# Kernel optimization log

Measured on AMD Instinct MI355X. Metric: run time of the kernel, lower is better.

## Reference

```python
import jax, jax.numpy as jnp
import numpy as np

N = 100000      # nodes (single node type)
E = 400000      # edges per relation
R = 4           # relations
DIN = 128       # h_dim
H1 = 8          # heads, layer 1
DH1 = DIN // H1 # per-head dim, layer 1
DOUT = 128      # out_dim (layer 2 has 1 head of dim DOUT)
NEG_SLOPE = 0.2 # GATConv default leaky_relu slope


def gat_rel_layer(h, src, dst, W, al, ar, loop_w, bias, activation):
    """One RelationalAttLayer: per-relation GATConv (bias=False), summed across
    relations, + self-loop matmul + bias + optional relu. dropout=0.
    h: [N, din]; src/dst: [R, E]; W: [R, din, H*Dh]; al/ar: [R, H, Dh];
    loop_w: [din, dout]; bias: [dout]."""
    n = h.shape[0]

    def per_rel(src_r, dst_r, W_r, al_r, ar_r):
        nh, dh = al_r.shape
        Wh = (h @ W_r).reshape(n, nh, dh)                 # [N,H,Dh]
        el = jnp.sum(Wh * al_r, axis=-1)                  # [N,H]
        er = jnp.sum(Wh * ar_r, axis=-1)                  # [N,H]
        e = jax.nn.leaky_relu(el[src_r] + er[dst_r], NEG_SLOPE)  # [E,H]
        # edge-softmax over incoming edges per destination node (stable)
        m = jax.lax.stop_gradient(jax.ops.segment_max(e, dst_r, num_segments=n))
        ex = jnp.exp(e - m[dst_r])
        denom = jax.ops.segment_sum(ex, dst_r, num_segments=n)  # [N,H]
        alpha = ex / denom[dst_r]                                # [E,H]
        # scatter-aggregate messages
        return jax.ops.segment_sum(alpha[:, :, None] * Wh[src_r], dst_r,
                                   num_segments=n)               # [N,H,Dh]

    outs = jax.vmap(per_rel)(src, dst, W, al, ar)  # [R,N,H,Dh]
    hout = outs.sum(0).reshape(n, -1)              # cross-relation sum, flatten heads
    hout = hout + h @ loop_w + bias                # self-loop + h_bias
    if activation:
        hout = jax.nn.relu(hout)
    return hout


def setup_inputs() -> dict:
    key = jax.random.key(0)
    ks = jax.random.split(key, 14)
    s = 0.1
    return {
        "h": jax.random.normal(ks[0], (N, DIN), dtype=jnp.float32),
        "src_idx": jax.random.randint(ks[1], (R, E), 0, N, dtype=jnp.int32),
        "dst_idx": jax.random.randint(ks[2], (R, E), 0, N, dtype=jnp.int32),
        # layer 1 params (h_dim -> h_dim, H1 heads)
        "W1": jax.random.normal(ks[3], (R, DIN, H1 * DH1), dtype=jnp.float32) * s,
        "al1": jax.random.normal(ks[4], (R, H1, DH1), dtype=jnp.float32) * s,
        "ar1": jax.random.normal(ks[5], (R, H1, DH1), dtype=jnp.float32) * s,
        "loop1": jax.random.normal(ks[6], (DIN, DIN), dtype=jnp.float32) * s,
        "b1": jnp.zeros((DIN,), dtype=jnp.float32),
        # layer 2 params (h_dim -> out_dim, 1 head)
        "W2": jax.random.normal(ks[7], (R, DIN, DOUT), dtype=jnp.float32) * s,
        "al2": jax.random.normal(ks[8], (R, 1, DOUT), dtype=jnp.float32) * s,
        "ar2": jax.random.normal(ks[9], (R, 1, DOUT), dtype=jnp.float32) * s,
        "loop2": jax.random.normal(ks[10], (DIN, DOUT), dtype=jnp.float32) * s,
        "b2": jnp.zeros((DOUT,), dtype=jnp.float32),
    }


def reference(h, src_idx, dst_idx, W1, al1, ar1, loop1, b1,
              W2, al2, ar2, loop2, b2):
    # hidden layer: relu activation; last layer: no activation (last_layer_act=False)
    h1 = gat_rel_layer(h, src_idx, dst_idx, W1, al1, ar1, loop1, b1, activation=True)
    h2 = gat_rel_layer(h1, src_idx, dst_idx, W2, al2, ar2, loop2, b2, activation=False)
    return h2
```

## Files before the change

### kernel.cpp

```cpp
#include <hip/hip_runtime.h>

#define NN 100000
#define NE 400000
#define NREL 4
#define MAXDEG 24

typedef unsigned short u16;
typedef __attribute__((ext_vector_type(8))) short bf16x8;
typedef __attribute__((ext_vector_type(4))) float f32x4;

__device__ __forceinline__ u16 f2bf(float x) {
    union { float f; unsigned int u; } v; v.f = x;
    unsigned int r = v.u + 0x7fffu + ((v.u >> 16) & 1u);
    return (u16)(r >> 16);
}
__device__ __forceinline__ float bf2f(u16 x) {
    union { unsigned int u; float f; } v; v.u = ((unsigned int)x) << 16;
    return v.f;
}

template <bool RELU>
__global__ __launch_bounds__(256) void conv_kernel(
    const float* __restrict__ X, u16* __restrict__ Xb, int n8)
{
    int i = blockIdx.x * 256 + threadIdx.x;
    if (i >= n8) return;
    float4 a = ((const float4*)X)[2 * i];
    float4 b = ((const float4*)X)[2 * i + 1];
    if (RELU) {
        a.x = fmaxf(a.x, 0.f); a.y = fmaxf(a.y, 0.f);
        a.z = fmaxf(a.z, 0.f); a.w = fmaxf(a.w, 0.f);
        b.x = fmaxf(b.x, 0.f); b.y = fmaxf(b.y, 0.f);
        b.z = fmaxf(b.z, 0.f); b.w = fmaxf(b.w, 0.f);
    }
    ushort4 lo, hi;
    lo.x = f2bf(a.x); lo.y = f2bf(a.y); lo.z = f2bf(a.z); lo.w = f2bf(a.w);
    hi.x = f2bf(b.x); hi.y = f2bf(b.y); hi.z = f2bf(b.z); hi.w = f2bf(b.w);
    ((ushort4*)Xb)[2 * i] = lo;
    ((ushort4*)Xb)[2 * i + 1] = hi;
}

__global__ __launch_bounds__(256) void build_b_kernel(
    const float* __restrict__ W, const float* __restrict__ loopw,
    u16* __restrict__ Bb)
{
    int id = blockIdx.x * 256 + threadIdx.x;
    if (id >= 5 * 16384) return;
    int j = id >> 14, rem = id & 16383;
    int c = rem >> 7, k = rem & 127;
    const float* M = (j < 4) ? (W + j * 16384) : loopw;
    Bb[id] = f2bf(M[k * 128 + c]);
}

__global__ __launch_bounds__(256) void build_w_kernel(
    const float* __restrict__ W, const float* __restrict__ al,
    const float* __restrict__ ar, u16* __restrict__ wcatB,
    int nh, int dh, int PC)
{
    int id = blockIdx.x * 256 + threadIdx.x;
    if (id >= PC * 128) return;
    int j = id >> 7, k = id & 127;
    int P2 = 8 * nh;
    float s = 0.f;
    if (j < P2) {
        int half = 4 * nh;
        int jj = (j < half) ? j : j - half;
        const float* av = (j < half) ? al : ar;
        int r = jj / nh, h = jj % nh;
        for (int i = 0; i < dh; ++i)
            s += W[r * 16384 + k * 128 + h * dh + i] * av[(r * nh + h) * dh + i];
    }
    wcatB[j * 128 + k] = f2bf(s);
}

__global__ __launch_bounds__(256) void csr_build_kernel(
    const int* __restrict__ src, const int* __restrict__ dst,
    int* __restrict__ cur, int* __restrict__ bucket)
{
    int i = blockIdx.x * 256 + threadIdx.x;
    if (i >= NREL * NE) return;
    int d = dst[i], s = src[i];
    int r = i / NE;
    int pos = atomicAdd(&cur[r * NN + d], 1);
    if (pos < MAXDEG) bucket[((size_t)r * NN + d) * MAXDEG + pos] = s;
}

__device__ __forceinline__ void stage_and_mfma(
    const u16* __restrict__ Xb, const u16* __restrict__ B, int row0, int n,
    u16 (*sA)[136], u16 (*sB)[136], f32x4 acc[8], int tid)
{
#pragma unroll
    for (int i = 0; i < 8; ++i) {
        int idx = tid + 256 * i;
        int r = idx >> 4, ch = idx & 15;
        *(float4*)&sB[r][ch * 8] = ((const float4*)B)[idx];
    }
#pragma unroll
    for (int i = 0; i < 4; ++i) {
        int idx = tid + 256 * i;
        int r = idx >> 4, ch = idx & 15;
        int gr = row0 + r;
        float4 v = make_float4(0.f, 0.f, 0.f, 0.f);
        if (gr < n) v = *(const float4*)(Xb + (size_t)gr * 128 + ch * 8);
        *(float4*)&sA[r][ch * 8] = v;
    }
    __syncthreads();

    const int w = tid >> 6, lane = tid & 63;
    const int lr = lane & 15, hi = lane >> 4;
#pragma unroll
    for (int fn = 0; fn < 8; ++fn) acc[fn] = (f32x4){0.f, 0.f, 0.f, 0.f};
#pragma unroll
    for (int ko = 0; ko < 4; ++ko) {
        const int kk = ko * 32 + hi * 8;
        bf16x8 a = *(const bf16x8*)&sA[w * 16 + lr][kk];
#pragma unroll
        for (int fn = 0; fn < 8; ++fn) {
            bf16x8 b = *(const bf16x8*)&sB[fn * 16 + lr][kk];
            acc[fn] = __builtin_amdgcn_mfma_f32_16x16x32_bf16(a, b, acc[fn], 0, 0, 0);
        }
    }
}

__global__ __launch_bounds__(256) void gemm_rel_kernel(
    const u16* __restrict__ Xb, const u16* __restrict__ Bb, int rbase,
    u16* __restrict__ Wh, int n)
{
    __shared__ u16 sA[64][136];
    __shared__ u16 sB[128][136];
    const int tid = threadIdx.x;
    const int row0 = blockIdx.x * 64;
    f32x4 acc[8];
    stage_and_mfma(Xb, Bb + (size_t)(rbase + blockIdx.y) * 16384, row0, n, sA, sB, acc, tid);

    const int w = tid >> 6, lane = tid & 63;
    const int lr = lane & 15, hi = lane >> 4;
    u16* Wr = Wh + (size_t)blockIdx.y * NN * 128;
#pragma unroll
    for (int reg = 0; reg < 4; ++reg) {
        int grow = row0 + w * 16 + hi * 4 + reg;
        if (grow >= n) continue;
        u16* crow = Wr + (size_t)grow * 128;
#pragma unroll
        for (int fn = 0; fn < 8; ++fn)
            crow[fn * 16 + lr] = f2bf(acc[fn][reg]);
    }
}

__global__ __launch_bounds__(256) void gemm_loop_kernel(
    const u16* __restrict__ Xb, const u16* __restrict__ Bb,
    float* __restrict__ O, const float* __restrict__ bias, int n)
{
    __shared__ u16 sA[64][136];
    __shared__ u16 sB[128][136];
    const int tid = threadIdx.x;
    const int row0 = blockIdx.x * 64;
    f32x4 acc[8];
    stage_and_mfma(Xb, Bb + 4 * 16384, row0, n, sA, sB, acc, tid);

    const int w = tid >> 6, lane = tid & 63;
    const int lr = lane & 15, hi = lane >> 4;
#pragma unroll
    for (int reg = 0; reg < 4; ++reg) {
        int grow = row0 + w * 16 + hi * 4 + reg;
        if (grow >= n) continue;
        float* crow = O + (size_t)grow * 128;
#pragma unroll
        for (int fn = 0; fn < 8; ++fn) {
            int col = fn * 16 + lr;
            crow[col] = acc[fn][reg] + bias[col];
        }
    }
}

template <int NF>
__global__ __launch_bounds__(256) void elr_gemm_kernel(
    const u16* __restrict__ Xb, const u16* __restrict__ Bb,
    float* __restrict__ Eo, int P2, int n)
{
    __shared__ u16 sA[64][136];
    __shared__ u16 sB[NF * 16][136];
    const int tid = threadIdx.x;
    const int row0 = blockIdx.x * 64;

    for (int idx = tid; idx < NF * 256; idx += 256) {
        int r = idx >> 4, ch = idx & 15;
        *(float4*)&sB[r][ch * 8] = ((const float4*)Bb)[idx];
    }
#pragma unroll
    for (int i = 0; i < 4; ++i) {
        int idx = tid + 256 * i;
        int r = idx >> 4, ch = idx & 15;
        int gr = row0 + r;
        float4 v = make_float4(0.f, 0.f, 0.f, 0.f);
        if (gr < n) v = *(const float4*)(Xb + (size_t)gr * 128 + ch * 8);
        *(float4*)&sA[r][ch * 8] = v;
    }
    __syncthreads();

    const int w = tid >> 6, lane = tid & 63;
    const int lr = lane & 15, hi = lane >> 4;
    f32x4 acc[NF];
#pragma unroll
    for (int fn = 0; fn < NF; ++fn) acc[fn] = (f32x4){0.f, 0.f, 0.f, 0.f};
#pragma unroll
    for (int ko = 0; ko < 4; ++ko) {
        const int kk = ko * 32 + hi * 8;
        bf16x8 a = *(const bf16x8*)&sA[w * 16 + lr][kk];
#pragma unroll
        for (int fn = 0; fn < NF; ++fn) {
            bf16x8 b = *(const bf16x8*)&sB[fn * 16 + lr][kk];
            acc[fn] = __builtin_amdgcn_mfma_f32_16x16x32_bf16(a, b, acc[fn], 0, 0, 0);
        }
    }
#pragma unroll
    for (int reg = 0; reg < 4; ++reg) {
        int grow = row0 + w * 16 + hi * 4 + reg;
        if (grow >= n) continue;
#pragma unroll
        for (int fn = 0; fn < NF; ++fn) {
            int col = fn * 16 + lr;
            if (col < P2) Eo[(size_t)grow * P2 + col] = acc[fn][reg];
        }
    }
}

__global__ __launch_bounds__(256) void gather_kernel(
    const int* __restrict__ cnt, const int* __restrict__ bucket,
    const float* __restrict__ elr, const u16* __restrict__ Wh,
    float* __restrict__ O, int ST, int nh, int dh_shift, int r0, int nb)
{
    int d = blockIdx.x * 4 + (threadIdx.x >> 6);
    if (d >= NN) return;
    int lane = threadIdx.x & 63;
    int c0 = lane * 2;
    int hh = c0 >> dh_shift;
    float M0 = 0.f, M1 = 0.f;
    for (int rr = 0; rr < nb; ++rr) {
        int r = r0 + rr;
        int deg = cnt[r * NN + d];
        if (deg <= 0) continue;
        deg = deg > MAXDEG ? MAXDEG : deg;
        const int* bk = bucket + ((size_t)r * NN + d) * MAXDEG;
        float erd = elr[(size_t)d * ST + NREL * nh + r * nh + hh];
        const u16* whr = Wh + (size_t)rr * NN * 128;
        float dn = 0.f, m0 = 0.f, m1 = 0.f;
        for (int e = 0; e < deg; ++e) {
            int s = bk[e];
            float v = elr[(size_t)s * ST + r * nh + hh] + erd;
            v = v > 0.f ? v : 0.2f * v;
            float ex = __expf(v);
            dn += ex;
            ushort2 wv = *(const ushort2*)(whr + (size_t)s * 128 + c0);
            m0 = fmaf(ex, bf2f(wv.x), m0);
            m1 = fmaf(ex, bf2f(wv.y), m1);
        }
        float inv = 1.f / dn;
        M0 = fmaf(m0, inv, M0);
        M1 = fmaf(m1, inv, M1);
    }
    float2* op = (float2*)(O + (size_t)d * 128) + lane;
    float2 c = *op;
    c.x += M0; c.y += M1;
    *op = c;
}

static void run_layer(const u16* Xb, float* O, const float* W,
                      const float* al, const float* ar, const float* loopw,
                      const float* biasv, int nh, int dh, int dh_shift, int NF,
                      const int* cnt, const int* bucket,
                      u16* Wh, float* elr, u16* Bb, u16* wcatB, int nb,
                      hipStream_t stream)
{
    const int P2 = 8 * nh, PC = NF * 16;
    build_b_kernel<<<(5 * 16384) / 256, 256, 0, stream>>>(W, loopw, Bb);
    build_w_kernel<<<(PC * 128 + 255) / 256, 256, 0, stream>>>(W, al, ar, wcatB, nh, dh, PC);

    const int gg = (NN + 63) / 64;
    gemm_loop_kernel<<<gg, 256, 0, stream>>>(Xb, Bb, O, biasv, NN);
    if (NF == 4)
        elr_gemm_kernel<4><<<gg, 256, 0, stream>>>(Xb, wcatB, elr, P2, NN);
    else
        elr_gemm_kernel<1><<<gg, 256, 0, stream>>>(Xb, wcatB, elr, P2, NN);

    for (int r0 = 0; r0 < NREL; r0 += nb) {
        gemm_rel_kernel<<<dim3(gg, nb), 256, 0, stream>>>(Xb, Bb, r0, Wh, NN);
        gather_kernel<<<(NN + 3) / 4, 256, 0, stream>>>(
            cnt, bucket, elr, Wh, O, P2, nh, dh_shift, r0, nb);
    }
}

extern "C" void kernel_launch(void* const* d_in, const int* in_sizes, int n_in,
                              void* d_out, int out_size, void* d_ws, size_t ws_size,
                              hipStream_t stream)
{
    const float* h   = (const float*)d_in[0];
    const int*   src = (const int*)d_in[1];
    const int*   dst = (const int*)d_in[2];
    const float* W1  = (const float*)d_in[3];
    const float* al1 = (const float*)d_in[4];
    const float* ar1 = (const float*)d_in[5];
    const float* lp1 = (const float*)d_in[6];
    const float* b1  = (const float*)d_in[7];
    const float* W2  = (const float*)d_in[8];
    const float* al2 = (const float*)d_in[9];
    const float* ar2 = (const float*)d_in[10];
    const float* lp2 = (const float*)d_in[11];
    const float* b2  = (const float*)d_in[12];

    float* out = (float*)d_out;
    char*  p   = (char*)d_ws;

    const size_t szXb  = (size_t)NN * 128 * 2;
    const size_t szO   = (size_t)NN * 128 * 4;
    const size_t szElr = (size_t)NN * 64 * 4;
    const size_t szCnt = (size_t)NREL * NN * 4;
    const size_t szBkt = (size_t)NREL * NN * MAXDEG * 4;
    const size_t szBb  = 5 * 16384 * 2;
    const size_t szWc  = 64 * 128 * 2;
    const size_t szWh1 = (size_t)NN * 128 * 2;
    const size_t fixed = szXb + szO + szElr + szCnt + szBkt + szBb + szWc;

    int nb = 1;
    if (ws_size >= fixed + 4 * szWh1) nb = 4;
    else if (ws_size >= fixed + 2 * szWh1) nb = 2;

    u16*   Xb     = (u16*)p;    p += szXb;
    float* O1     = (float*)p;  p += szO;
    float* elr    = (float*)p;  p += szElr;
    int*   cnt    = (int*)p;    p += szCnt;
    int*   bucket = (int*)p;    p += szBkt;
    u16*   Bb     = (u16*)p;    p += szBb;
    u16*   wcatB  = (u16*)p;    p += szWc;
    u16*   Wh     = (u16*)p;

    hipMemsetAsync(cnt, 0, szCnt, stream);
    csr_build_kernel<<<(NREL * NE + 255) / 256, 256, 0, stream>>>(src, dst, cnt, bucket);

    const int n8 = NN * 128 / 8;
    conv_kernel<false><<<(n8 + 255) / 256, 256, 0, stream>>>(h, Xb, n8);
    run_layer(Xb, O1, W1, al1, ar1, lp1, b1, 8, 16, 4, 4,
              cnt, bucket, Wh, elr, Bb, wcatB, nb, stream);
    conv_kernel<true><<<(n8 + 255) / 256, 256, 0, stream>>>(O1, Xb, n8);
    run_layer(Xb, out, W2, al2, ar2, lp2, b2, 1, 128, 7, 1,
              cnt, bucket, Wh, elr, Bb, wcatB, nb, stream);
}
```

Measured before the change: 821.1 us.

## Fuse per-layer GEMMs into one launch and parallelize gather across relations

The relation, self-loop and attention-logit GEMMs now run in a single kernel with a 6-way grid y dimension, replacing several launches. The gather kernel gives each destination node its own block, with one wave per relation and a shared-memory reduction, and unrolls the edge loop by four with vectorized index loads. CSR construction handles all four relations per thread. The workspace-size fallback for fewer relation buffers is removed, so the code always assumes room for all four Wh buffers; this risks failure when the workspace is small, and the gather launches more, smaller blocks.

```diff
diff --git a/kernel.cpp b/kernel.cpp
--- a/kernel.cpp
+++ b/kernel.cpp
@@ -54,11 +54,10 @@
 
 __global__ __launch_bounds__(256) void build_w_kernel(
     const float* __restrict__ W, const float* __restrict__ al,
-    const float* __restrict__ ar, u16* __restrict__ wcatB,
-    int nh, int dh, int PC)
+    const float* __restrict__ ar, u16* __restrict__ wcatB, int nh, int dh)
 {
     int id = blockIdx.x * 256 + threadIdx.x;
-    if (id >= PC * 128) return;
+    if (id >= 16384) return;
     int j = id >> 7, k = id & 127;
     int P2 = 8 * nh;
     float s = 0.f;
@@ -78,22 +77,39 @@
     int* __restrict__ cur, int* __restrict__ bucket)
 {
     int i = blockIdx.x * 256 + threadIdx.x;
-    if (i >= NREL * NE) return;
-    int d = dst[i], s = src[i];
-    int r = i / NE;
-    int pos = atomicAdd(&cur[r * NN + d], 1);
-    if (pos < MAXDEG) bucket[((size_t)r * NN + d) * MAXDEG + pos] = s;
-}
-
-__device__ __forceinline__ void stage_and_mfma(
-    const u16* __restrict__ Xb, const u16* __restrict__ B, int row0, int n,
-    u16 (*sA)[136], u16 (*sB)[136], f32x4 acc[8], int tid)
-{
+    if (i >= NE) return;
+    int d0 = dst[i],          s0 = src[i];
+    int d1 = dst[NE + i],     s1 = src[NE + i];
+    int d2 = dst[2 * NE + i], s2 = src[2 * NE + i];
+    int d3 = dst[3 * NE + i], s3 = src[3 * NE + i];
+    int p0 = atomicAdd(&cur[d0], 1);
+    int p1 = atomicAdd(&cur[NN + d1], 1);
+    int p2 = atomicAdd(&cur[2 * NN + d2], 1);
+    int p3 = atomicAdd(&cur[3 * NN + d3], 1);
+    if (p0 < MAXDEG) bucket[(size_t)d0 * MAXDEG + p0] = s0;
+    if (p1 < MAXDEG) bucket[((size_t)NN + d1) * MAXDEG + p1] = s1;
+    if (p2 < MAXDEG) bucket[((size_t)2 * NN + d2) * MAXDEG + p2] = s2;
+    if (p3 < MAXDEG) bucket[((size_t)3 * NN + d3) * MAXDEG + p3] = s3;
+}
+
+__global__ __launch_bounds__(256) void fused_gemm_kernel(
+    const u16* __restrict__ Xb, const u16* __restrict__ Bb,
+    const u16* __restrict__ wcatB, u16* __restrict__ Wh,
+    float* __restrict__ O, const float* __restrict__ bias,
+    float* __restrict__ elr, int P2, int n)
+{
+    __shared__ u16 sA[64][136];
+    __shared__ u16 sB[128][136];
+    const int tid = threadIdx.x;
+    const int y = blockIdx.y;
+    const int row0 = blockIdx.x * 64;
+    const u16* Bmat = (y < 5) ? (Bb + (size_t)y * 16384) : wcatB;
+
 #pragma unroll
     for (int i = 0; i < 8; ++i) {
         int idx = tid + 256 * i;
         int r = idx >> 4, ch = idx & 15;
-        *(float4*)&sB[r][ch * 8] = ((const float4*)B)[idx];
+        *(float4*)&sB[r][ch * 8] = ((const float4*)Bmat)[idx];
     }
 #pragma unroll
     for (int i = 0; i < 4; ++i) {
@@ -108,6 +124,7 @@
 
     const int w = tid >> 6, lane = tid & 63;
     const int lr = lane & 15, hi = lane >> 4;
+    f32x4 acc[8];
 #pragma unroll
     for (int fn = 0; fn < 8; ++fn) acc[fn] = (f32x4){0.f, 0.f, 0.f, 0.f};
 #pragma unroll
@@ -120,107 +137,40 @@
             acc[fn] = __builtin_amdgcn_mfma_f32_16x16x32_bf16(a, b, acc[fn], 0, 0, 0);
         }
     }
-}
-
-__global__ __launch_bounds__(256) void gemm_rel_kernel(
-    const u16* __restrict__ Xb, const u16* __restrict__ Bb, int rbase,
-    u16* __restrict__ Wh, int n)
-{
-    __shared__ u16 sA[64][136];
-    __shared__ u16 sB[128][136];
-    const int tid = threadIdx.x;
-    const int row0 = blockIdx.x * 64;
-    f32x4 acc[8];
-    stage_and_mfma(Xb, Bb + (size_t)(rbase + blockIdx.y) * 16384, row0, n, sA, sB, acc, tid);
-
-    const int w = tid >> 6, lane = tid & 63;
-    const int lr = lane & 15, hi = lane >> 4;
-    u16* Wr = Wh + (size_t)blockIdx.y * NN * 128;
-#pragma unroll
-    for (int reg = 0; reg < 4; ++reg) {
-        int grow = row0 + w * 16 + hi * 4 + reg;
-        if (grow >= n) continue;
-        u16* crow = Wr + (size_t)grow * 128;
-#pragma unroll
-        for (int fn = 0; fn < 8; ++fn)
-            crow[fn * 16 + lr] = f2bf(acc[fn][reg]);
-    }
-}
-
-__global__ __launch_bounds__(256) void gemm_loop_kernel(
-    const u16* __restrict__ Xb, const u16* __restrict__ Bb,
-    float* __restrict__ O, const float* __restrict__ bias, int n)
-{
-    __shared__ u16 sA[64][136];
-    __shared__ u16 sB[128][136];
-    const int tid = threadIdx.x;
-    const int row0 = blockIdx.x * 64;
-    f32x4 acc[8];
-    stage_and_mfma(Xb, Bb + 4 * 16384, row0, n, sA, sB, acc, tid);
-
-    const int w = tid >> 6, lane = tid & 63;
-    const int lr = lane & 15, hi = lane >> 4;
-#pragma unroll
-    for (int reg = 0; reg < 4; ++reg) {
-        int grow = row0 + w * 16 + hi * 4 + reg;
-        if (grow >= n) continue;
-        float* crow = O + (size_t)grow * 128;
-#pragma unroll
-        for (int fn = 0; fn < 8; ++fn) {
-            int col = fn * 16 + lr;
-            crow[col] = acc[fn][reg] + bias[col];
-        }
-    }
-}
-
-template <int NF>
-__global__ __launch_bounds__(256) void elr_gemm_kernel(
-    const u16* __restrict__ Xb, const u16* __restrict__ Bb,
-    float* __restrict__ Eo, int P2, int n)
-{
-    __shared__ u16 sA[64][136];
-    __shared__ u16 sB[NF * 16][136];
-    const int tid = threadIdx.x;
-    const int row0 = blockIdx.x * 64;
-
-    for (int idx = tid; idx < NF * 256; idx += 256) {
-        int r = idx >> 4, ch = idx & 15;
-        *(float4*)&sB[r][ch * 8] = ((const float4*)Bb)[idx];
-    }
-#pragma unroll
-    for (int i = 0; i < 4; ++i) {
-        int idx = tid + 256 * i;
-        int r = idx >> 4, ch = idx & 15;
-        int gr = row0 + r;
-        float4 v = make_float4(0.f, 0.f, 0.f, 0.f);
-        if (gr < n) v = *(const float4*)(Xb + (size_t)gr * 128 + ch * 8);
-        *(float4*)&sA[r][ch * 8] = v;
-    }
-    __syncthreads();
-
-    const int w = tid >> 6, lane = tid & 63;
-    const int lr = lane & 15, hi = lane >> 4;
-    f32x4 acc[NF];
-#pragma unroll
-    for (int fn = 0; fn < NF; ++fn) acc[fn] = (f32x4){0.f, 0.f, 0.f, 0.f};
-#pragma unroll
-    for (int ko = 0; ko < 4; ++ko) {
-        const int kk = ko * 32 + hi * 8;
-        bf16x8 a = *(const bf16x8*)&sA[w * 16 + lr][kk];
-#pragma unroll
-        for (int fn = 0; fn < NF; ++fn) {
-            bf16x8 b = *(const bf16x8*)&sB[fn * 16 + lr][kk];
-            acc[fn] = __builtin_amdgcn_mfma_f32_16x16x32_bf16(a, b, acc[fn], 0, 0, 0);
-        }
-    }
-#pragma unroll
-    for (int reg = 0; reg < 4; ++reg) {
-        int grow = row0 + w * 16 + hi * 4 + reg;
-        if (grow >= n) continue;
-#pragma unroll
-        for (int fn = 0; fn < NF; ++fn) {
-            int col = fn * 16 + lr;
-            if (col < P2) Eo[(size_t)grow * P2 + col] = acc[fn][reg];
+
+    if (y < 4) {
+        u16* Wr = Wh + (size_t)y * NN * 128;
+#pragma unroll
+        for (int reg = 0; reg < 4; ++reg) {
+            int grow = row0 + w * 16 + hi * 4 + reg;
+            if (grow >= n) continue;
+            u16* crow = Wr + (size_t)grow * 128;
+#pragma unroll
+            for (int fn = 0; fn < 8; ++fn)
+                crow[fn * 16 + lr] = f2bf(acc[fn][reg]);
+        }
+    } else if (y == 4) {
+#pragma unroll
+        for (int reg = 0; reg < 4; ++reg) {
+            int grow = row0 + w * 16 + hi * 4 + reg;
+            if (grow >= n) continue;
+            float* crow = O + (size_t)grow * 128;
+#pragma unroll
+            for (int fn = 0; fn < 8; ++fn) {
+                int col = fn * 16 + lr;
+                crow[col] = acc[fn][reg] + bias[col];
+            }
+        }
+    } else {
+#pragma unroll
+        for (int reg = 0; reg < 4; ++reg) {
+            int grow = row0 + w * 16 + hi * 4 + reg;
+            if (grow >= n) continue;
+#pragma unroll
+            for (int fn = 0; fn < 8; ++fn) {
+                int col = fn * 16 + lr;
+                if (col < P2) elr[(size_t)grow * P2 + col] = acc[fn][reg];
+            }
         }
     }
 }
@@ -228,66 +178,86 @@
 __global__ __launch_bounds__(256) void gather_kernel(
     const int* __restrict__ cnt, const int* __restrict__ bucket,
     const float* __restrict__ elr, const u16* __restrict__ Wh,
-    float* __restrict__ O, int ST, int nh, int dh_shift, int r0, int nb)
-{
-    int d = blockIdx.x * 4 + (threadIdx.x >> 6);
-    if (d >= NN) return;
-    int lane = threadIdx.x & 63;
-    int c0 = lane * 2;
-    int hh = c0 >> dh_shift;
+    float* __restrict__ O, int ST, int nh, int dh_shift)
+{
+    const int d = blockIdx.x;
+    const int w = threadIdx.x >> 6;
+    const int lane = threadIdx.x & 63;
+    const int c0 = lane * 2;
+    const int hh = c0 >> dh_shift;
+    __shared__ float2 part[4][64];
+
     float M0 = 0.f, M1 = 0.f;
-    for (int rr = 0; rr < nb; ++rr) {
-        int r = r0 + rr;
-        int deg = cnt[r * NN + d];
-        if (deg <= 0) continue;
-        deg = deg > MAXDEG ? MAXDEG : deg;
-        const int* bk = bucket + ((size_t)r * NN + d) * MAXDEG;
-        float erd = elr[(size_t)d * ST + NREL * nh + r * nh + hh];
-        const u16* whr = Wh + (size_t)rr * NN * 128;
+    int deg = cnt[w * NN + d];
+    deg = deg > MAXDEG ? MAXDEG : deg;
+    if (deg > 0) {
+        const int* bk = bucket + ((size_t)w * NN + d) * MAXDEG;
+        const float erd = elr[(size_t)d * ST + NREL * nh + w * nh + hh];
+        const u16* whr = Wh + (size_t)w * NN * 128;
+        const int eo = w * nh + hh;
         float dn = 0.f, m0 = 0.f, m1 = 0.f;
-        for (int e = 0; e < deg; ++e) {
+        int e = 0;
+        for (; e + 4 <= deg; e += 4) {
+            int4 q = *(const int4*)(bk + e);
+            float va = elr[(size_t)q.x * ST + eo];
+            float vb = elr[(size_t)q.y * ST + eo];
+            float vc = elr[(size_t)q.z * ST + eo];
+            float vd = elr[(size_t)q.w * ST + eo];
+            ushort2 wa = *(const ushort2*)(whr + (size_t)q.x * 128 + c0);
+            ushort2 wb = *(const ushort2*)(whr + (size_t)q.y * 128 + c0);
+            ushort2 wc = *(const ushort2*)(whr + (size_t)q.z * 128 + c0);
+            ushort2 wd = *(const ushort2*)(whr + (size_t)q.w * 128 + c0);
+            float v, ex;
+            v = va + erd; v = v > 0.f ? v : 0.2f * v; ex = __expf(v);
+            dn += ex; m0 = fmaf(ex, bf2f(wa.x), m0); m1 = fmaf(ex, bf2f(wa.y), m1);
+            v = vb + erd; v = v > 0.f ? v : 0.2f * v; ex = __expf(v);
+            dn += ex; m0 = fmaf(ex, bf2f(wb.x), m0); m1 = fmaf(ex, bf2f(wb.y), m1);
+            v = vc + erd; v = v > 0.f ? v : 0.2f * v; ex = __expf(v);
+            dn += ex; m0 = fmaf(ex, bf2f(wc.x), m0); m1 = fmaf(ex, bf2f(wc.y), m1);
+            v = vd + erd; v = v > 0.f ? v : 0.2f * v; ex = __expf(v);
+            dn += ex; m0 = fmaf(ex, bf2f(wd.x), m0); m1 = fmaf(ex, bf2f(wd.y), m1);
+        }
+        for (; e < deg; ++e) {
             int s = bk[e];
-            float v = elr[(size_t)s * ST + r * nh + hh] + erd;
+            float v = elr[(size_t)s * ST + eo] + erd;
             v = v > 0.f ? v : 0.2f * v;
             float ex = __expf(v);
+            ushort2 wv = *(const ushort2*)(whr + (size_t)s * 128 + c0);
             dn += ex;
-            ushort2 wv = *(const ushort2*)(whr + (size_t)s * 128 + c0);
             m0 = fmaf(ex, bf2f(wv.x), m0);
             m1 = fmaf(ex, bf2f(wv.y), m1);
         }
         float inv = 1.f / dn;
-        M0 = fmaf(m0, inv, M0);
-        M1 = fmaf(m1, inv, M1);
-    }
-    float2* op = (float2*)(O + (size_t)d * 128) + lane;
-    float2 c = *op;
-    c.x += M0; c.y += M1;
-    *op = c;
+        M0 = m0 * inv; M1 = m1 * inv;
+    }
+    part[w][lane] = make_float2(M0, M1);
+    __syncthreads();
+    if (w == 0) {
+        float2 a = part[0][lane], b = part[1][lane];
+        float2 c = part[2][lane], e4 = part[3][lane];
+        float2* op = (float2*)(O + (size_t)d * 128) + lane;
+        float2 cc = *op;
+        cc.x += a.x + b.x + c.x + e4.x;
+        cc.y += a.y + b.y + c.y + e4.y;
+        *op = cc;
+    }
 }
 
 static void run_layer(const u16* Xb, float* O, const float* W,
                       const float* al, const float* ar, const float* loopw,
-                      const float* biasv, int nh, int dh, int dh_shift, int NF,
+                      const float* biasv, int nh, int dh, int dh_shift,
                       const int* cnt, const int* bucket,
-                      u16* Wh, float* elr, u16* Bb, u16* wcatB, int nb,
+                      u16* Wh, float* elr, u16* Bb, u16* wcatB,
                       hipStream_t stream)
 {
-    const int P2 = 8 * nh, PC = NF * 16;
+    const int P2 = 8 * nh;
     build_b_kernel<<<(5 * 16384) / 256, 256, 0, stream>>>(W, loopw, Bb);
-    build_w_kernel<<<(PC * 128 + 255) / 256, 256, 0, stream>>>(W, al, ar, wcatB, nh, dh, PC);
+    build_w_kernel<<<16384 / 256, 256, 0, stream>>>(W, al, ar, wcatB, nh, dh);
 
     const int gg = (NN + 63) / 64;
-    gemm_loop_kernel<<<gg, 256, 0, stream>>>(Xb, Bb, O, biasv, NN);
-    if (NF == 4)
-        elr_gemm_kernel<4><<<gg, 256, 0, stream>>>(Xb, wcatB, elr, P2, NN);
-    else
-        elr_gemm_kernel<1><<<gg, 256, 0, stream>>>(Xb, wcatB, elr, P2, NN);
-
-    for (int r0 = 0; r0 < NREL; r0 += nb) {
-        gemm_rel_kernel<<<dim3(gg, nb), 256, 0, stream>>>(Xb, Bb, r0, Wh, NN);
-        gather_kernel<<<(NN + 3) / 4, 256, 0, stream>>>(
-            cnt, bucket, elr, Wh, O, P2, nh, dh_shift, r0, nb);
-    }
+    fused_gemm_kernel<<<dim3(gg, 6), 256, 0, stream>>>(
+        Xb, Bb, wcatB, Wh, O, biasv, elr, P2, NN);
+    gather_kernel<<<NN, 256, 0, stream>>>(cnt, bucket, elr, Wh, O, P2, nh, dh_shift);
 }
 
 extern "C" void kernel_launch(void* const* d_in, const int* in_sizes, int n_in,
@@ -317,13 +287,7 @@
     const size_t szCnt = (size_t)NREL * NN * 4;
     const size_t szBkt = (size_t)NREL * NN * MAXDEG * 4;
     const size_t szBb  = 5 * 16384 * 2;
-    const size_t szWc  = 64 * 128 * 2;
-    const size_t szWh1 = (size_t)NN * 128 * 2;
-    const size_t fixed = szXb + szO + szElr + szCnt + szBkt + szBb + szWc;
-
-    int nb = 1;
-    if (ws_size >= fixed + 4 * szWh1) nb = 4;
-    else if (ws_size >= fixed + 2 * szWh1) nb = 2;
+    const size_t szWc  = 16384 * 2;
 
     u16*   Xb     = (u16*)p;    p += szXb;
     float* O1     = (float*)p;  p += szO;
@@ -335,13 +299,13 @@
     u16*   Wh     = (u16*)p;
 
     hipMemsetAsync(cnt, 0, szCnt, stream);
-    csr_build_kernel<<<(NREL * NE + 255) / 256, 256, 0, stream>>>(src, dst, cnt, bucket);
+    csr_build_kernel<<<(NE + 255) / 256, 256, 0, stream>>>(src, dst, cnt, bucket);
 
     const int n8 = NN * 128 / 8;
     conv_kernel<false><<<(n8 + 255) / 256, 256, 0, stream>>>(h, Xb, n8);
-    run_layer(Xb, O1, W1, al1, ar1, lp1, b1, 8, 16, 4, 4,
-              cnt, bucket, Wh, elr, Bb, wcatB, nb, stream);
+    run_layer(Xb, O1, W1, al1, ar1, lp1, b1, 8, 16, 4,
+              cnt, bucket, Wh, elr, Bb, wcatB, stream);
     conv_kernel<true><<<(n8 + 255) / 256, 256, 0, stream>>>(O1, Xb, n8);
-    run_layer(Xb, out, W2, al2, ar2, lp2, b2, 1, 128, 7, 1,
-              cnt, bucket, Wh, elr, Bb, wcatB, nb, stream);
-}
+    run_layer(Xb, out, W2, al2, ar2, lp2, b2, 1, 128, 7,
+              cnt, bucket, Wh, elr, Bb, wcatB, stream);
+}
```

Measured after the change: 760.1 us. 7.4% less time.
